# Optimization experiments

Hardware: AMD Instinct MI355X
Metric: run time of the kernel (lower is better)

Reference implementation:

```python
import jax, jax.numpy as jnp
import numpy as np

EPS = 1e-5
K = 3  # kernel size
K2 = K * K
PAD = 1


def conv2d(x, w, b):
    # x: [B,C,H,W], w: [O,C,3,3], b: [O]
    y = jax.lax.conv_general_dilated(
        x, w, window_strides=(1, 1), padding=((PAD, PAD), (PAD, PAD)),
        dimension_numbers=("NCHW", "OIHW", "NCHW"))
    return y + b[None, :, None, None]


def bilinear_sample(x, py, px):
    # x: [B,C,H,W]; py,px: [B,K2,H,W] fractional sample coords (zero pad outside)
    B, C, H, W = x.shape
    y0 = jnp.floor(py)
    x0 = jnp.floor(px)
    wy1 = py - y0
    wx1 = px - x0
    wy0 = 1.0 - wy1
    wx0 = 1.0 - wx1
    xf = x.reshape(B, C, H * W)

    def gather(yy, xx):
        valid = ((yy >= 0) & (yy < H) & (xx >= 0) & (xx < W)).astype(x.dtype)
        yc = jnp.clip(yy, 0, H - 1).astype(jnp.int32)
        xc = jnp.clip(xx, 0, W - 1).astype(jnp.int32)
        idx = yc * W + xc  # [B,K2,H,W]
        v = jax.vmap(lambda f, i: f[:, i])(xf, idx)  # [B,C,K2,H,W]
        return v * valid[:, None]

    out = (wy0 * wx0)[:, None] * gather(y0, x0)
    out = out + (wy0 * wx1)[:, None] * gather(y0, x0 + 1)
    out = out + (wy1 * wx0)[:, None] * gather(y0 + 1, x0)
    out = out + (wy1 * wx1)[:, None] * gather(y0 + 1, x0 + 1)
    return out  # [B,C,K2,H,W]


def deform_conv2d(x, offset_w, offset_b, w, b):
    # Deformable conv v1: offsets predicted by a plain 3x3 conv, then
    # bilinear gather at (base grid + kernel tap + learned offset),
    # contracted against the conv weight.
    B, C, H, W = x.shape
    O = w.shape[0]
    off = conv2d(x, offset_w, offset_b)            # [B, 2*K2, H, W]
    off = off.reshape(B, K2, 2, H, W)
    dy, dx = off[:, :, 0], off[:, :, 1]            # [B,K2,H,W]
    ky = (jnp.arange(K2) // K - PAD).astype(x.dtype)[None, :, None, None]
    kx = (jnp.arange(K2) % K - PAD).astype(x.dtype)[None, :, None, None]
    ii = jnp.arange(H, dtype=x.dtype)[None, None, :, None]
    jj = jnp.arange(W, dtype=x.dtype)[None, None, None, :]
    py = ii + ky + dy
    px = jj + kx + dx
    sampled = bilinear_sample(x, py, px)           # [B,C,K2,H,W]
    out = jnp.einsum("bckhw,ock->bohw", sampled, w.reshape(O, C, K2))
    return out + b[None, :, None, None]


def group_norm(x, gamma, beta):
    # num_groups=1: normalize over (C,H,W) per sample
    mean = jnp.mean(x, axis=(1, 2, 3), keepdims=True)
    var = jnp.var(x, axis=(1, 2, 3), keepdims=True)
    xn = (x - mean) * jax.lax.rsqrt(var + EPS)
    return xn * gamma[None, :, None, None] + beta[None, :, None, None]


def setup_inputs() -> dict:
    key = jax.random.key(0)
    ks = jax.random.split(key, 8)
    B, C, H, W = 4, 256, 64, 64
    s = 1.0 / np.sqrt(C * K2)
    inp = {
        "x": jax.random.normal(ks[0], (B, C, H, W), jnp.float32),
        "ow1": jax.random.normal(ks[1], (2 * K2, C, K, K), jnp.float32) * 0.01,
        "ob1": jnp.zeros((2 * K2,), jnp.float32),
        "dw1": jax.random.normal(ks[2], (C, C, K, K), jnp.float32) * s,
        "db1": jax.random.normal(ks[3], (C,), jnp.float32) * 0.01,
        "g1": jnp.ones((C,), jnp.float32),
        "b1": jnp.zeros((C,), jnp.float32),
        "ow2": jax.random.normal(ks[4], (2 * K2, C, K, K), jnp.float32) * 0.01,
        "ob2": jnp.zeros((2 * K2,), jnp.float32),
        "dw2": jax.random.normal(ks[5], (C, C, K, K), jnp.float32) * s,
        "db2": jax.random.normal(ks[6], (C,), jnp.float32) * 0.01,
        "g2": jnp.ones((C,), jnp.float32),
        "b2": jnp.zeros((C,), jnp.float32),
        "g3": jnp.ones((C,), jnp.float32),
        "b3": jnp.zeros((C,), jnp.float32),
    }
    return inp


def reference(x, ow1, ob1, dw1, db1, g1, b1,
              ow2, ob2, dw2, db2, g2, b2, g3, b3):
    # block: deform_conv -> GN -> relu -> (dropout=id in eval) x2
    h = jax.nn.relu(group_norm(deform_conv2d(x, ow1, ob1, dw1, db1), g1, b1))
    h = jax.nn.relu(group_norm(deform_conv2d(h, ow2, ob2, dw2, db2), g2, b2))
    # drop_path=0 -> identity; in_channels == out_channels -> identity shortcut
    return group_norm(h + x, g3, b3)
```

## Files before the change

kernel.cpp:

```cpp
#include <hip/hip_runtime.h>
#include <hip/hip_fp16.h>

constexpr int B = 4, C = 256, H = 64, W = 64, HW = 4096;
constexpr int K2 = 9, OFFC = 18;
constexpr int SSTR = 296;

typedef short s16x8 __attribute__((ext_vector_type(8)));
typedef float f32x4 __attribute__((ext_vector_type(4)));

__device__ __forceinline__ unsigned short f2bf(float f) {
  unsigned u = __float_as_uint(f);
  u += 0x7fffu + ((u >> 16) & 1u);
  return (unsigned short)(u >> 16);
}
__device__ __forceinline__ float bflo(unsigned q) { return __uint_as_float(q << 16); }
__device__ __forceinline__ float bfhi(unsigned q) { return __uint_as_float(q & 0xffff0000u); }

__global__ void cvt_bf16_reord_k(const float* __restrict__ src, unsigned short* __restrict__ dst) {
  int idx = blockIdx.x * 256 + threadIdx.x;
  if (idx >= 256 * 2304) return;
  int o = idx / 2304, kap = idx % 2304;
  int cbi = kap / 288, rem = kap % 288;
  int k = rem >> 5, c = rem & 31;
  dst[idx] = f2bf(src[((size_t)(o * 256 + cbi * 32 + c)) * 9 + k]);
}

__launch_bounds__(256)
__global__ void offset_conv_k(const float* __restrict__ x, const float* __restrict__ ow,
                              const float* __restrict__ ob, float* __restrict__ off4) {
  int cq = blockIdx.x & 3;
  int i  = (blockIdx.x >> 2) & 63;
  int b  = blockIdx.x >> 8;
  int t = threadIdx.x;
  int j = t & 63;
  int ocg = __builtin_amdgcn_readfirstlane(t >> 6);
  __shared__ float xs[32][3][66];
  const float* xb = x + (size_t)b * C * HW;

  if (t < 96) { int cc = t & 31, rr = t >> 5; xs[cc][rr][0] = 0.f; xs[cc][rr][65] = 0.f; }

  float acc[5];
#pragma unroll
  for (int s = 0; s < 5; ++s) {
    int oc = ocg + 4 * s;
    acc[s] = (cq == 0 && oc < OFFC) ? ob[oc] : 0.f;
  }

  for (int half = 0; half < 2; ++half) {
    int cbase = cq * 64 + half * 32;
    for (int idx = t; idx < 32 * 192; idx += 256) {
      int cc = idx / 192, rem = idx - cc * 192;
      int rr = rem >> 6, j2 = rem & 63;
      int yy = i + rr - 1;
      xs[cc][rr][1 + j2] = (yy >= 0 && yy < H) ? xb[(size_t)(cbase + cc) * HW + yy * 64 + j2] : 0.f;
    }
    __syncthreads();
    for (int cc = 0; cc < 32; ++cc) {
      float xv[9];
#pragma unroll
      for (int rr = 0; rr < 3; ++rr)
#pragma unroll
        for (int dxx = 0; dxx < 3; ++dxx) xv[rr * 3 + dxx] = xs[cc][rr][j + dxx];
#pragma unroll
      for (int s = 0; s < 5; ++s) {
        int oc = ocg + 4 * s;
        if (oc < OFFC) {
          const float* wp = ow + ((size_t)oc * C + cbase + cc) * 9;
#pragma unroll
          for (int k = 0; k < 9; ++k) acc[s] += xv[k] * wp[k];
        }
      }
    }
    __syncthreads();
  }
#pragma unroll
  for (int s = 0; s < 5; ++s) {
    int oc = ocg + 4 * s;
    if (oc < OFFC)
      off4[(((size_t)(cq * B + b) * OFFC + oc) << 12) + (i << 6) + j] = acc[s];
  }
}

__launch_bounds__(512, 4)
__global__ void deform_mfma_k(const float* __restrict__ xin, const float* __restrict__ off4,
                              const unsigned short* __restrict__ wbf,
                              const float* __restrict__ bias,
                              float* __restrict__ y, float* __restrict__ stats) {
  int jh = blockIdx.x & 1;
  int i  = (blockIdx.x >> 1) & 63;
  int b  = blockIdx.x >> 7;
  int t = threadIdx.x;
  int lane = t & 63, wv = t >> 6;
  int cidx = lane & 15, r = lane >> 4;
  int jl = t & 31, cg = t >> 5;

  __shared__ __align__(16) unsigned s_md[K2][32][4];
  __shared__ __align__(16) unsigned short s_pt[2][11264];
  __shared__ __align__(16) unsigned short s_s[32][SSTR];
  __shared__ float rs_[8], rq_[8];

  const float* xb = xin + (size_t)b * C * HW;
  int br = i - 3, bc = (jh << 5) - 5;

  int gof[11], wof[11];
#pragma unroll
  for (int e = 0; e < 11; ++e) {
    int pos = jl + (e << 5);
    int row = pos / 44, col = pos - row * 44;
    int rr = min(max(br + row, 0), H - 1);
    int c2 = min(max(bc + col, 0), W - 1);
    gof[e] = rr * 64 + c2;
    wof[e] = cg * 704 + row * 88 + col * 2;
  }

  float l0[11], l1[11];
  {
    const float* bp = xb + (size_t)(cg * 2) * HW;
#pragma unroll
    for (int e = 0; e < 11; ++e) { l0[e] = bp[gof[e]]; l1[e] = bp[HW + gof[e]]; }
  }

  for (int idx = t; idx < K2 * 32; idx += 512) {
    int k = idx >> 5, jj = idx & 31;
    int j = (jh << 5) + jj;
    float dy = 0.f, dx = 0.f;
#pragma unroll
    for (int cq = 0; cq < 4; ++cq) {
      const float* p = off4 + (((size_t)(cq * B + b) * OFFC) << 12) + (i << 6) + j;
      dy += p[(2 * k) << 12];
      dx += p[(2 * k + 1) << 12];
    }
    float py = (float)(i + (k / 3) - 1) + dy;
    float px = (float)(j + (k % 3) - 1) + dx;
    float y0f = floorf(py), x0f = floorf(px);
    float wy1 = py - y0f, wx1 = px - x0f;
    float wy0 = 1.f - wy1, wx0 = 1.f - wx1;
    int y0 = (int)y0f, x0 = (int)x0f;
    if (y0 < 0 || y0 >= H)         wy0 = 0.f;
    if (y0 + 1 < 0 || y0 + 1 >= H) wy1 = 0.f;
    if (x0 < 0 || x0 >= W)         wx0 = 0.f;
    if (x0 + 1 < 0 || x0 + 1 >= W) wx1 = 0.f;
    int y0c = min(max(y0, 0), H - 1), y1c = min(max(y0 + 1, 0), H - 1);
    int x0c = min(max(x0, 0), W - 1), x1c = min(max(x0 + 1, 0), W - 1);
    int dys = y1c - y0c, dxs = x1c - x0c;
    unsigned p0 = (unsigned)__half_as_ushort(__float2half_rn(wy0 * wx0)) |
                  ((unsigned)__half_as_ushort(__float2half_rn(wy0 * wx1)) << 16);
    unsigned p1 = (unsigned)__half_as_ushort(__float2half_rn(wy1 * wx0)) |
                  ((unsigned)__half_as_ushort(__float2half_rn(wy1 * wx1)) << 16);
    bool ip = (y0c >= br) && (y1c <= br + 7) && (x0c >= bc) && (x1c <= bc + 43);
    unsigned pb = (unsigned)((y0c - br) * 88 + (x0c - bc) * 2);
    unsigned p2 = (ip ? (pb & 0xfff) : 0u) | ((unsigned)dxs << 12) | ((unsigned)dys << 13) |
                  (ip ? 0u : 0x4000u);
    unsigned p3 = (unsigned)(y0c * 64 + x0c) | ((unsigned)dxs << 12) | ((unsigned)dys << 13);
    *reinterpret_cast<uint4*>(&s_md[k][jj][0]) = make_uint4(p0, p1, p2, p3);
  }

#pragma unroll
  for (int e = 0; e < 11; ++e)
    *reinterpret_cast<unsigned*>(&s_pt[0][wof[e]]) =
        (unsigned)f2bf(l0[e]) | ((unsigned)f2bf(l1[e]) << 16);
  __syncthreads();

  f32x4 acc[2][2];
#pragma unroll
  for (int m = 0; m < 2; ++m) {
    acc[m][0] = {0.f, 0.f, 0.f, 0.f};
    acc[m][1] = {0.f, 0.f, 0.f, 0.f};
  }
  int ob_ = wv * 32;
  const unsigned short* w0p = wbf + (size_t)(ob_ + cidx) * 2304;
  const unsigned short* w1p = w0p + 16 * 2304;

  for (int cb = 0; cb < 8; ++cb) {
    int cur = cb & 1;
    if (cb < 7) {
      const float* bp = xb + (size_t)((cb + 1) * 32 + cg * 2) * HW;
#pragma unroll
      for (int e = 0; e < 11; ++e) { l0[e] = bp[gof[e]]; l1[e] = bp[HW + gof[e]]; }
    }
    {
      const unsigned short* pt = &s_pt[cur][cg * 704];
#pragma unroll
      for (int k = 0; k < K2; ++k) {
        uint4 m = *reinterpret_cast<const uint4*>(&s_md[k][jl][0]);
        float w00 = __half2float(__ushort_as_half((unsigned short)(m.x & 0xffff)));
        float w01 = __half2float(__ushort_as_half((unsigned short)(m.x >> 16)));
        float w10 = __half2float(__ushort_as_half((unsigned short)(m.y & 0xffff)));
        float w11 = __half2float(__ushort_as_half((unsigned short)(m.y >> 16)));
        int pb = m.z & 0xfff;
        int dx2 = ((m.z >> 12) & 1) * 2, dy88 = ((m.z >> 13) & 1) * 88;
        unsigned q00 = *reinterpret_cast<const unsigned*>(pt + pb);
        unsigned q01 = *reinterpret_cast<const unsigned*>(pt + pb + dx2);
        unsigned q10 = *reinterpret_cast<const unsigned*>(pt + pb + dy88);
        unsigned q11 = *reinterpret_cast<const unsigned*>(pt + pb + dy88 + dx2);
        float v0 = w00 * bflo(q00) + w01 * bflo(q01) + w10 * bflo(q10) + w11 * bflo(q11);
        float v1 = w00 * bfhi(q00) + w01 * bfhi(q01) + w10 * bfhi(q10) + w11 * bfhi(q11);
        if (m.z & 0x4000u) {
          int i00 = m.w & 0xfff;
          int fdx = (m.w >> 12) & 1, fdy = ((m.w >> 13) & 1) * 64;
          const float* xc0 = xb + (size_t)(cb * 32 + cg * 2) * HW;
          const float* xc1 = xc0 + HW;
          v0 = w00 * xc0[i00] + w01 * xc0[i00 + fdx] + w10 * xc0[i00 + fdy] + w11 * xc0[i00 + fdy + fdx];
          v1 = w00 * xc1[i00] + w01 * xc1[i00 + fdx] + w10 * xc1[i00 + fdy] + w11 * xc1[i00 + fdy + fdx];
        }
        *reinterpret_cast<unsigned*>(&s_s[jl][k * 32 + cg * 2]) =
            (unsigned)f2bf(v0) | ((unsigned)f2bf(v1) << 16);
      }
    }
    if (cb < 7) {
#pragma unroll
      for (int e = 0; e < 11; ++e)
        *reinterpret_cast<unsigned*>(&s_pt[cur ^ 1][wof[e]]) =
            (unsigned)f2bf(l0[e]) | ((unsigned)f2bf(l1[e]) << 16);
    }
    __syncthreads();
    int kb0 = cb * 288 + r * 8;
#pragma unroll 3
    for (int kk = 0; kk < 9; ++kk) {
      int kl = kk * 32 + r * 8;
      s16x8 a0 = *(const s16x8*)&s_s[cidx][kl];
      s16x8 a1 = *(const s16x8*)&s_s[16 + cidx][kl];
      s16x8 b0 = *(const s16x8*)&w0p[kb0 + kk * 32];
      s16x8 b1 = *(const s16x8*)&w1p[kb0 + kk * 32];
      acc[0][0] = __builtin_amdgcn_mfma_f32_16x16x32_bf16(a0, b0, acc[0][0], 0, 0, 0);
      acc[1][0] = __builtin_amdgcn_mfma_f32_16x16x32_bf16(a1, b0, acc[1][0], 0, 0, 0);
      acc[0][1] = __builtin_amdgcn_mfma_f32_16x16x32_bf16(a0, b1, acc[0][1], 0, 0, 0);
      acc[1][1] = __builtin_amdgcn_mfma_f32_16x16x32_bf16(a1, b1, acc[1][1], 0, 0, 0);
    }
    __syncthreads();
  }

  float bv0 = bias[ob_ + cidx], bv1 = bias[ob_ + 16 + cidx];
  float psum = 0.f, psq = 0.f;
#pragma unroll
  for (int m = 0; m < 2; ++m) {
#pragma unroll
    for (int n = 0; n < 2; ++n) {
      int o = ob_ + n * 16 + cidx;
      float bv = n ? bv1 : bv0;
      float4 vv;
      vv.x = acc[m][n][0] + bv; vv.y = acc[m][n][1] + bv;
      vv.z = acc[m][n][2] + bv; vv.w = acc[m][n][3] + bv;
      *reinterpret_cast<float4*>(y + (((size_t)(b * C + o)) << 12) + (i << 6) + (jh << 5) + m * 16 + r * 4) = vv;
      psum += vv.x + vv.y + vv.z + vv.w;
      psq  += vv.x * vv.x + vv.y * vv.y + vv.z * vv.z + vv.w * vv.w;
    }
  }
#pragma unroll
  for (int d = 32; d > 0; d >>= 1) {
    psum += __shfl_down(psum, d);
    psq  += __shfl_down(psq, d);
  }
  if (lane == 0) { rs_[wv] = psum; rq_[wv] = psq; }
  __syncthreads();
  if (t == 0) {
    float a = 0.f, s2 = 0.f;
    for (int u = 0; u < 8; ++u) { a += rs_[u]; s2 += rq_[u]; }
    atomicAdd(&stats[b * 2],     a);
    atomicAdd(&stats[b * 2 + 1], s2);
  }
}

__global__ void gn_k(const float* __restrict__ yv, const float* __restrict__ stats,
                     const float* __restrict__ g, const float* __restrict__ be,
                     float* __restrict__ outp, int relu) {
  const float inv = 1.f / (float)(C * HW);
  int stride = gridDim.x * blockDim.x;
  int total4 = B * C * HW / 4;
  for (int idx = blockIdx.x * blockDim.x + threadIdx.x; idx < total4; idx += stride) {
    int e = idx << 2;
    int b = e >> 20;
    int c = (e >> 12) & 255;
    float mean = stats[b * 2] * inv;
    float var  = stats[b * 2 + 1] * inv - mean * mean;
    float rs   = rsqrtf(var + 1e-5f);
    float a  = g[c] * rs;
    float b2 = be[c] - mean * a;
    float4 v = *reinterpret_cast<const float4*>(yv + e);
    float4 rr;
    rr.x = v.x * a + b2; rr.y = v.y * a + b2; rr.z = v.z * a + b2; rr.w = v.w * a + b2;
    if (relu) {
      rr.x = fmaxf(0.f, rr.x); rr.y = fmaxf(0.f, rr.y);
      rr.z = fmaxf(0.f, rr.z); rr.w = fmaxf(0.f, rr.w);
    }
    *reinterpret_cast<float4*>(outp + e) = rr;
  }
}

__global__ void res_stats_k(const float* __restrict__ h2, const float* __restrict__ x,
                            float* __restrict__ z, float* __restrict__ stats) {
  int b = blockIdx.x >> 8;
  int seg = blockIdx.x & 255;
  size_t base = ((size_t)b << 20) + ((size_t)seg << 12);
  int t = threadIdx.x;
  float psum = 0.f, psq = 0.f;
#pragma unroll
  for (int u = 0; u < 4; ++u) {
    size_t e = base + (size_t)(u * 256 + t) * 4;
    float4 a = *reinterpret_cast<const float4*>(h2 + e);
    float4 c = *reinterpret_cast<const float4*>(x + e);
    float4 rr = make_float4(a.x + c.x, a.y + c.y, a.z + c.z, a.w + c.w);
    *reinterpret_cast<float4*>(z + e) = rr;
    psum += rr.x + rr.y + rr.z + rr.w;
    psq  += rr.x * rr.x + rr.y * rr.y + rr.z * rr.z + rr.w * rr.w;
  }
#pragma unroll
  for (int d = 32; d > 0; d >>= 1) {
    psum += __shfl_down(psum, d);
    psq  += __shfl_down(psq, d);
  }
  __shared__ float rs_[4], rq_[4];
  int wid = t >> 6, lane = t & 63;
  if (lane == 0) { rs_[wid] = psum; rq_[wid] = psq; }
  __syncthreads();
  if (t == 0) {
    float a = 0.f, s2 = 0.f;
    for (int u = 0; u < 4; ++u) { a += rs_[u]; s2 += rq_[u]; }
    atomicAdd(&stats[b * 2],     a);
    atomicAdd(&stats[b * 2 + 1], s2);
  }
}

extern "C" void kernel_launch(void* const* d_in, const int* in_sizes, int n_in,
                              void* d_out, int out_size, void* d_ws, size_t ws_size,
                              hipStream_t stream) {
  const float* x   = (const float*)d_in[0];
  const float* ow1 = (const float*)d_in[1];
  const float* ob1 = (const float*)d_in[2];
  const float* dw1 = (const float*)d_in[3];
  const float* db1 = (const float*)d_in[4];
  const float* g1  = (const float*)d_in[5];
  const float* b1  = (const float*)d_in[6];
  const float* ow2 = (const float*)d_in[7];
  const float* ob2 = (const float*)d_in[8];
  const float* dw2 = (const float*)d_in[9];
  const float* db2 = (const float*)d_in[10];
  const float* g2  = (const float*)d_in[11];
  const float* b2  = (const float*)d_in[12];
  const float* g3  = (const float*)d_in[13];
  const float* b3  = (const float*)d_in[14];

  float* ws   = (float*)d_ws;
  float* off4 = ws;
  float* yb   = ws + 1179648;
  float* hb   = ws + 1179648 + 4194304;
  float* st   = ws + 1179648 + 2 * 4194304;
  unsigned short* wbf1 = (unsigned short*)(ws + 9568288);
  unsigned short* wbf2 = (unsigned short*)(ws + 9568288 + 294912);
  float* outp = (float*)d_out;

  hipMemsetAsync(st, 0, 32 * sizeof(float), stream);
  cvt_bf16_reord_k<<<2304, 256, 0, stream>>>(dw1, wbf1);
  cvt_bf16_reord_k<<<2304, 256, 0, stream>>>(dw2, wbf2);

  offset_conv_k<<<1024, 256, 0, stream>>>(x, ow1, ob1, off4);
  deform_mfma_k<<<512, 512, 0, stream>>>(x, off4, wbf1, db1, yb, st + 0);
  gn_k<<<2048, 256, 0, stream>>>(yb, st + 0, g1, b1, hb, 1);
  offset_conv_k<<<1024, 256, 0, stream>>>(hb, ow2, ob2, off4);
  deform_mfma_k<<<512, 512, 0, stream>>>(hb, off4, wbf2, db2, yb, st + 8);
  gn_k<<<2048, 256, 0, stream>>>(yb, st + 8, g2, b2, hb, 1);
  res_stats_k<<<1024, 256, 0, stream>>>(hb, x, yb, st + 16);
  gn_k<<<2048, 256, 0, stream>>>(yb, st + 16, g3, b3, outp, 0);
}
```

Baseline: 474.0 us.

## Switch activations to packed fp16 channel pairs and fuse GN with residual

Activations are now stored as packed half2 channel pairs (x converted once, hidden h written packed by a GN+ReLU kernel). The offset conv and the bilinear sampling use packed half2 FMA, and the MFMA moves from bf16 to f16. The second GN+ReLU is fused with the residual add and the stats pass. This cuts memory traffic and ALU work in the sampling and offset conv, at the cost of fp16 range and precision in the offset conv accumulation and the bilinear interpolation.

```diff
diff --git a/kernel.cpp b/kernel.cpp
--- a/kernel.cpp
+++ b/kernel.cpp
@@ -3,30 +3,46 @@
 
 constexpr int B = 4, C = 256, H = 64, W = 64, HW = 4096;
 constexpr int K2 = 9, OFFC = 18;
-constexpr int SSTR = 296;
-
-typedef short s16x8 __attribute__((ext_vector_type(8)));
+constexpr int PSTR = 356;
+
+typedef _Float16 f16x8 __attribute__((ext_vector_type(8)));
 typedef float f32x4 __attribute__((ext_vector_type(4)));
 
-__device__ __forceinline__ unsigned short f2bf(float f) {
-  unsigned u = __float_as_uint(f);
-  u += 0x7fffu + ((u >> 16) & 1u);
-  return (unsigned short)(u >> 16);
-}
-__device__ __forceinline__ float bflo(unsigned q) { return __uint_as_float(q << 16); }
-__device__ __forceinline__ float bfhi(unsigned q) { return __uint_as_float(q & 0xffff0000u); }
-
-__global__ void cvt_bf16_reord_k(const float* __restrict__ src, unsigned short* __restrict__ dst) {
+__device__ __forceinline__ __half2 u2h(unsigned u) { return *reinterpret_cast<__half2*>(&u); }
+__device__ __forceinline__ unsigned h2u(__half2 h) { return *reinterpret_cast<unsigned*>(&h); }
+__device__ __forceinline__ unsigned packh2(float a, float b) {
+  __half2 h = __floats2half2_rn(a, b);
+  return *reinterpret_cast<unsigned*>(&h);
+}
+
+__global__ void cvt_wf16_reord_k(const float* __restrict__ src, __half* __restrict__ dst) {
   int idx = blockIdx.x * 256 + threadIdx.x;
   if (idx >= 256 * 2304) return;
   int o = idx / 2304, kap = idx % 2304;
   int cbi = kap / 288, rem = kap % 288;
   int k = rem >> 5, c = rem & 31;
-  dst[idx] = f2bf(src[((size_t)(o * 256 + cbi * 32 + c)) * 9 + k]);
+  dst[idx] = __float2half_rn(src[((size_t)(o * 256 + cbi * 32 + c)) * 9 + k]);
+}
+
+__global__ void cvt_owpair_k(const float* __restrict__ src, unsigned* __restrict__ dst) {
+  int idx = blockIdx.x * 256 + threadIdx.x;
+  if (idx >= OFFC * 128 * 9) return;
+  int k = idx % 9, cp = (idx / 9) & 127, oc = idx / 1152;
+  dst[idx] = packh2(src[((size_t)oc * 256 + 2 * cp) * 9 + k],
+                    src[((size_t)oc * 256 + 2 * cp + 1) * 9 + k]);
+}
+
+__global__ void cvt_xpair_k(const float* __restrict__ src, unsigned* __restrict__ dst) {
+  int idx = blockIdx.x * 256 + threadIdx.x;
+  int px4 = idx & 1023, c2 = (idx >> 10) & 127, b = idx >> 17;
+  const float4 v0 = *reinterpret_cast<const float4*>(src + (((size_t)(b * 256 + 2 * c2)) << 12) + px4 * 4);
+  const float4 v1 = *reinterpret_cast<const float4*>(src + (((size_t)(b * 256 + 2 * c2 + 1)) << 12) + px4 * 4);
+  uint4 o = make_uint4(packh2(v0.x, v1.x), packh2(v0.y, v1.y), packh2(v0.z, v1.z), packh2(v0.w, v1.w));
+  *reinterpret_cast<uint4*>(dst + (((size_t)(b * 128 + c2)) << 12) + px4 * 4) = o;
 }
 
 __launch_bounds__(256)
-__global__ void offset_conv_k(const float* __restrict__ x, const float* __restrict__ ow,
+__global__ void offset_conv_k(const unsigned* __restrict__ xp, const unsigned* __restrict__ owp,
                               const float* __restrict__ ob, float* __restrict__ off4) {
   int cq = blockIdx.x & 3;
   int i  = (blockIdx.x >> 2) & 63;
@@ -34,10 +50,19 @@
   int t = threadIdx.x;
   int j = t & 63;
   int ocg = __builtin_amdgcn_readfirstlane(t >> 6);
-  __shared__ float xs[32][3][66];
-  const float* xb = x + (size_t)b * C * HW;
-
-  if (t < 96) { int cc = t & 31, rr = t >> 5; xs[cc][rr][0] = 0.f; xs[cc][rr][65] = 0.f; }
+  __shared__ unsigned xs[32][3][66];
+  const unsigned* xb = xp + (size_t)b * 128 * HW;
+
+  for (int pos = t; pos < 32 * 3 * 66; pos += 256) {
+    int c = pos % 66, rp = pos / 66;
+    int rr = rp % 3, p = rp / 3;
+    int yy = i + rr - 1, xx = c - 1;
+    unsigned v = 0;
+    if (yy >= 0 && yy < H && xx >= 0 && xx < W)
+      v = xb[(size_t)(cq * 32 + p) * HW + yy * 64 + xx];
+    xs[p][rr][c] = v;
+  }
+  __syncthreads();
 
   float acc[5];
 #pragma unroll
@@ -46,32 +71,24 @@
     acc[s] = (cq == 0 && oc < OFFC) ? ob[oc] : 0.f;
   }
 
-  for (int half = 0; half < 2; ++half) {
-    int cbase = cq * 64 + half * 32;
-    for (int idx = t; idx < 32 * 192; idx += 256) {
-      int cc = idx / 192, rem = idx - cc * 192;
-      int rr = rem >> 6, j2 = rem & 63;
-      int yy = i + rr - 1;
-      xs[cc][rr][1 + j2] = (yy >= 0 && yy < H) ? xb[(size_t)(cbase + cc) * HW + yy * 64 + j2] : 0.f;
-    }
-    __syncthreads();
-    for (int cc = 0; cc < 32; ++cc) {
-      float xv[9];
-#pragma unroll
-      for (int rr = 0; rr < 3; ++rr)
-#pragma unroll
-        for (int dxx = 0; dxx < 3; ++dxx) xv[rr * 3 + dxx] = xs[cc][rr][j + dxx];
-#pragma unroll
-      for (int s = 0; s < 5; ++s) {
-        int oc = ocg + 4 * s;
-        if (oc < OFFC) {
-          const float* wp = ow + ((size_t)oc * C + cbase + cc) * 9;
-#pragma unroll
-          for (int k = 0; k < 9; ++k) acc[s] += xv[k] * wp[k];
-        }
+  for (int p = 0; p < 32; ++p) {
+    __half2 xv[9];
+#pragma unroll
+    for (int rr = 0; rr < 3; ++rr)
+#pragma unroll
+      for (int dxx = 0; dxx < 3; ++dxx) xv[rr * 3 + dxx] = u2h(xs[p][rr][j + dxx]);
+#pragma unroll
+    for (int s = 0; s < 5; ++s) {
+      int oc = ocg + 4 * s;
+      if (oc < OFFC) {
+        const unsigned* wp = owp + ((size_t)oc * 128 + cq * 32 + p) * 9;
+        __half2 h = __floats2half2_rn(0.f, 0.f);
+#pragma unroll
+        for (int k = 0; k < 9; ++k) h = __hfma2(xv[k], u2h(wp[k]), h);
+        float2 f = __half22float2(h);
+        acc[s] += f.x + f.y;
       }
     }
-    __syncthreads();
   }
 #pragma unroll
   for (int s = 0; s < 5; ++s) {
@@ -82,8 +99,8 @@
 }
 
 __launch_bounds__(512, 4)
-__global__ void deform_mfma_k(const float* __restrict__ xin, const float* __restrict__ off4,
-                              const unsigned short* __restrict__ wbf,
+__global__ void deform_mfma_k(const unsigned* __restrict__ xp, const float* __restrict__ off4,
+                              const __half* __restrict__ wf,
                               const float* __restrict__ bias,
                               float* __restrict__ y, float* __restrict__ stats) {
   int jh = blockIdx.x & 1;
@@ -95,11 +112,12 @@
   int jl = t & 31, cg = t >> 5;
 
   __shared__ __align__(16) unsigned s_md[K2][32][4];
-  __shared__ __align__(16) unsigned short s_pt[2][11264];
-  __shared__ __align__(16) unsigned short s_s[32][SSTR];
+  __shared__ __align__(8)  unsigned s_mf[K2][32][2];
+  __shared__ unsigned s_pt[2][16 * PSTR];
+  __shared__ __align__(16) unsigned s_su[32][148];
   __shared__ float rs_[8], rq_[8];
 
-  const float* xb = xin + (size_t)b * C * HW;
+  const unsigned* xb = xp + (size_t)b * 128 * HW;
   int br = i - 3, bc = (jh << 5) - 5;
 
   int gof[11], wof[11];
@@ -110,14 +128,14 @@
     int rr = min(max(br + row, 0), H - 1);
     int c2 = min(max(bc + col, 0), W - 1);
     gof[e] = rr * 64 + c2;
-    wof[e] = cg * 704 + row * 88 + col * 2;
-  }
-
-  float l0[11], l1[11];
+    wof[e] = row * 44 + col;
+  }
+
+  unsigned l[11];
   {
-    const float* bp = xb + (size_t)(cg * 2) * HW;
-#pragma unroll
-    for (int e = 0; e < 11; ++e) { l0[e] = bp[gof[e]]; l1[e] = bp[HW + gof[e]]; }
+    const unsigned* bp = xb + (size_t)cg * HW;
+#pragma unroll
+    for (int e = 0; e < 11; ++e) l[e] = bp[gof[e]];
   }
 
   for (int idx = t; idx < K2 * 32; idx += 512) {
@@ -143,23 +161,29 @@
     int y0c = min(max(y0, 0), H - 1), y1c = min(max(y0 + 1, 0), H - 1);
     int x0c = min(max(x0, 0), W - 1), x1c = min(max(x0 + 1, 0), W - 1);
     int dys = y1c - y0c, dxs = x1c - x0c;
-    unsigned p0 = (unsigned)__half_as_ushort(__float2half_rn(wy0 * wx0)) |
-                  ((unsigned)__half_as_ushort(__float2half_rn(wy0 * wx1)) << 16);
-    unsigned p1 = (unsigned)__half_as_ushort(__float2half_rn(wy1 * wx0)) |
-                  ((unsigned)__half_as_ushort(__float2half_rn(wy1 * wx1)) << 16);
+    uint4 wq;
+    wq.x = h2u(__float2half2_rn(wy0 * wx0));
+    wq.y = h2u(__float2half2_rn(wy0 * wx1));
+    wq.z = h2u(__float2half2_rn(wy1 * wx0));
+    wq.w = h2u(__float2half2_rn(wy1 * wx1));
+    *reinterpret_cast<uint4*>(&s_md[k][jj][0]) = wq;
     bool ip = (y0c >= br) && (y1c <= br + 7) && (x0c >= bc) && (x1c <= bc + 43);
-    unsigned pb = (unsigned)((y0c - br) * 88 + (x0c - bc) * 2);
-    unsigned p2 = (ip ? (pb & 0xfff) : 0u) | ((unsigned)dxs << 12) | ((unsigned)dys << 13) |
-                  (ip ? 0u : 0x4000u);
-    unsigned p3 = (unsigned)(y0c * 64 + x0c) | ((unsigned)dxs << 12) | ((unsigned)dys << 13);
-    *reinterpret_cast<uint4*>(&s_md[k][jj][0]) = make_uint4(p0, p1, p2, p3);
-  }
-
-#pragma unroll
-  for (int e = 0; e < 11; ++e)
-    *reinterpret_cast<unsigned*>(&s_pt[0][wof[e]]) =
-        (unsigned)f2bf(l0[e]) | ((unsigned)f2bf(l1[e]) << 16);
+    unsigned pb = (unsigned)((y0c - br) * 44 + (x0c - bc));
+    s_mf[k][jj][0] = (ip ? (pb & 0xfff) : 0u) | ((unsigned)dxs << 12) | ((unsigned)dys << 13) |
+                     (ip ? 0u : 0x4000u);
+    s_mf[k][jj][1] = (unsigned)(y0c * 64 + x0c) | ((unsigned)dxs << 12) | ((unsigned)dys << 13);
+  }
+
+#pragma unroll
+  for (int e = 0; e < 11; ++e) s_pt[0][cg * PSTR + wof[e]] = l[e];
   __syncthreads();
+
+  unsigned pbf[9], fbk[9];
+#pragma unroll
+  for (int k = 0; k < K2; ++k) {
+    uint2 mm = *reinterpret_cast<const uint2*>(&s_mf[k][jl][0]);
+    pbf[k] = mm.x; fbk[k] = mm.y;
+  }
 
   f32x4 acc[2][2];
 #pragma unroll
@@ -168,64 +192,59 @@
     acc[m][1] = {0.f, 0.f, 0.f, 0.f};
   }
   int ob_ = wv * 32;
-  const unsigned short* w0p = wbf + (size_t)(ob_ + cidx) * 2304;
-  const unsigned short* w1p = w0p + 16 * 2304;
+  const __half* w0p = wf + (size_t)(ob_ + cidx) * 2304;
+  const __half* w1p = w0p + 16 * 2304;
 
   for (int cb = 0; cb < 8; ++cb) {
     int cur = cb & 1;
     if (cb < 7) {
-      const float* bp = xb + (size_t)((cb + 1) * 32 + cg * 2) * HW;
-#pragma unroll
-      for (int e = 0; e < 11; ++e) { l0[e] = bp[gof[e]]; l1[e] = bp[HW + gof[e]]; }
+      const unsigned* bp = xb + (size_t)((cb + 1) * 16 + cg) * HW;
+#pragma unroll
+      for (int e = 0; e < 11; ++e) l[e] = bp[gof[e]];
     }
     {
-      const unsigned short* pt = &s_pt[cur][cg * 704];
+      const unsigned* pt = &s_pt[cur][cg * PSTR];
 #pragma unroll
       for (int k = 0; k < K2; ++k) {
         uint4 m = *reinterpret_cast<const uint4*>(&s_md[k][jl][0]);
-        float w00 = __half2float(__ushort_as_half((unsigned short)(m.x & 0xffff)));
-        float w01 = __half2float(__ushort_as_half((unsigned short)(m.x >> 16)));
-        float w10 = __half2float(__ushort_as_half((unsigned short)(m.y & 0xffff)));
-        float w11 = __half2float(__ushort_as_half((unsigned short)(m.y >> 16)));
-        int pb = m.z & 0xfff;
-        int dx2 = ((m.z >> 12) & 1) * 2, dy88 = ((m.z >> 13) & 1) * 88;
-        unsigned q00 = *reinterpret_cast<const unsigned*>(pt + pb);
-        unsigned q01 = *reinterpret_cast<const unsigned*>(pt + pb + dx2);
-        unsigned q10 = *reinterpret_cast<const unsigned*>(pt + pb + dy88);
-        unsigned q11 = *reinterpret_cast<const unsigned*>(pt + pb + dy88 + dx2);
-        float v0 = w00 * bflo(q00) + w01 * bflo(q01) + w10 * bflo(q10) + w11 * bflo(q11);
-        float v1 = w00 * bfhi(q00) + w01 * bfhi(q01) + w10 * bfhi(q10) + w11 * bfhi(q11);
-        if (m.z & 0x4000u) {
-          int i00 = m.w & 0xfff;
-          int fdx = (m.w >> 12) & 1, fdy = ((m.w >> 13) & 1) * 64;
-          const float* xc0 = xb + (size_t)(cb * 32 + cg * 2) * HW;
-          const float* xc1 = xc0 + HW;
-          v0 = w00 * xc0[i00] + w01 * xc0[i00 + fdx] + w10 * xc0[i00 + fdy] + w11 * xc0[i00 + fdy + fdx];
-          v1 = w00 * xc1[i00] + w01 * xc1[i00 + fdx] + w10 * xc1[i00 + fdy] + w11 * xc1[i00 + fdy + fdx];
+        unsigned z = pbf[k];
+        int pb = z & 0xfff;
+        int dxx = (z >> 12) & 1, dyy = ((z >> 13) & 1) ? 44 : 0;
+        __half2 q00 = u2h(pt[pb]),        q01 = u2h(pt[pb + dxx]);
+        __half2 q10 = u2h(pt[pb + dyy]),  q11 = u2h(pt[pb + dyy + dxx]);
+        __half2 v = __hmul2(u2h(m.x), q00);
+        v = __hfma2(u2h(m.y), q01, v);
+        v = __hfma2(u2h(m.z), q10, v);
+        v = __hfma2(u2h(m.w), q11, v);
+        if (z & 0x4000u) {
+          unsigned f = fbk[k];
+          int i00 = f & 0xfff;
+          int fdx = (f >> 12) & 1, fdy = ((f >> 13) & 1) ? 64 : 0;
+          const unsigned* xc = xb + (size_t)(cb * 16 + cg) * HW;
+          v = __hmul2(u2h(m.x), u2h(xc[i00]));
+          v = __hfma2(u2h(m.y), u2h(xc[i00 + fdx]), v);
+          v = __hfma2(u2h(m.z), u2h(xc[i00 + fdy]), v);
+          v = __hfma2(u2h(m.w), u2h(xc[i00 + fdy + fdx]), v);
         }
-        *reinterpret_cast<unsigned*>(&s_s[jl][k * 32 + cg * 2]) =
-            (unsigned)f2bf(v0) | ((unsigned)f2bf(v1) << 16);
+        s_su[jl][k * 16 + cg] = h2u(v);
       }
     }
     if (cb < 7) {
 #pragma unroll
-      for (int e = 0; e < 11; ++e)
-        *reinterpret_cast<unsigned*>(&s_pt[cur ^ 1][wof[e]]) =
-            (unsigned)f2bf(l0[e]) | ((unsigned)f2bf(l1[e]) << 16);
+      for (int e = 0; e < 11; ++e) s_pt[cur ^ 1][cg * PSTR + wof[e]] = l[e];
     }
     __syncthreads();
     int kb0 = cb * 288 + r * 8;
 #pragma unroll 3
     for (int kk = 0; kk < 9; ++kk) {
-      int kl = kk * 32 + r * 8;
-      s16x8 a0 = *(const s16x8*)&s_s[cidx][kl];
-      s16x8 a1 = *(const s16x8*)&s_s[16 + cidx][kl];
-      s16x8 b0 = *(const s16x8*)&w0p[kb0 + kk * 32];
-      s16x8 b1 = *(const s16x8*)&w1p[kb0 + kk * 32];
-      acc[0][0] = __builtin_amdgcn_mfma_f32_16x16x32_bf16(a0, b0, acc[0][0], 0, 0, 0);
-      acc[1][0] = __builtin_amdgcn_mfma_f32_16x16x32_bf16(a1, b0, acc[1][0], 0, 0, 0);
-      acc[0][1] = __builtin_amdgcn_mfma_f32_16x16x32_bf16(a0, b1, acc[0][1], 0, 0, 0);
-      acc[1][1] = __builtin_amdgcn_mfma_f32_16x16x32_bf16(a1, b1, acc[1][1], 0, 0, 0);
+      f16x8 a0 = *(const f16x8*)&s_su[cidx][kk * 16 + r * 4];
+      f16x8 a1 = *(const f16x8*)&s_su[16 + cidx][kk * 16 + r * 4];
+      f16x8 b0 = *(const f16x8*)&w0p[kb0 + kk * 32];
+      f16x8 b1 = *(const f16x8*)&w1p[kb0 + kk * 32];
+      acc[0][0] = __builtin_amdgcn_mfma_f32_16x16x32_f16(a0, b0, acc[0][0], 0, 0, 0);
+      acc[1][0] = __builtin_amdgcn_mfma_f32_16x16x32_f16(a1, b0, acc[1][0], 0, 0, 0);
+      acc[0][1] = __builtin_amdgcn_mfma_f32_16x16x32_f16(a0, b1, acc[0][1], 0, 0, 0);
+      acc[1][1] = __builtin_amdgcn_mfma_f32_16x16x32_f16(a1, b1, acc[1][1], 0, 0, 0);
     }
     __syncthreads();
   }
@@ -261,9 +280,76 @@
   }
 }
 
+__global__ void gn_pair_k(const float* __restrict__ yv, const float* __restrict__ stats,
+                          const float* __restrict__ g, const float* __restrict__ be,
+                          unsigned* __restrict__ outp) {
+  const float inv = 1.f / (float)(C * HW);
+  int idx = blockIdx.x * 256 + threadIdx.x;
+  int px4 = idx & 1023, c2 = (idx >> 10) & 127, b = idx >> 17;
+  float mean = stats[b * 2] * inv;
+  float var  = stats[b * 2 + 1] * inv - mean * mean;
+  float rs   = rsqrtf(var + 1e-5f);
+  float a0 = g[2 * c2] * rs,     bb0 = be[2 * c2] - mean * a0;
+  float a1 = g[2 * c2 + 1] * rs, bb1 = be[2 * c2 + 1] - mean * a1;
+  const float4 v0 = *reinterpret_cast<const float4*>(yv + (((size_t)(b * 256 + 2 * c2)) << 12) + px4 * 4);
+  const float4 v1 = *reinterpret_cast<const float4*>(yv + (((size_t)(b * 256 + 2 * c2 + 1)) << 12) + px4 * 4);
+  uint4 o;
+  o.x = packh2(fmaxf(0.f, v0.x * a0 + bb0), fmaxf(0.f, v1.x * a1 + bb1));
+  o.y = packh2(fmaxf(0.f, v0.y * a0 + bb0), fmaxf(0.f, v1.y * a1 + bb1));
+  o.z = packh2(fmaxf(0.f, v0.z * a0 + bb0), fmaxf(0.f, v1.z * a1 + bb1));
+  o.w = packh2(fmaxf(0.f, v0.w * a0 + bb0), fmaxf(0.f, v1.w * a1 + bb1));
+  *reinterpret_cast<uint4*>(outp + (((size_t)(b * 128 + c2)) << 12) + px4 * 4) = o;
+}
+
+__global__ void gn2res_k(const float* __restrict__ yv, const float* __restrict__ stats,
+                         const float* __restrict__ g, const float* __restrict__ be,
+                         const float* __restrict__ x, float* __restrict__ z,
+                         float* __restrict__ stats3) {
+  const float inv = 1.f / (float)(C * HW);
+  int b = blockIdx.x >> 8;
+  int seg = blockIdx.x & 255;
+  size_t base = ((size_t)b << 20) + ((size_t)seg << 12);
+  int t = threadIdx.x;
+  float mean = stats[b * 2] * inv;
+  float var  = stats[b * 2 + 1] * inv - mean * mean;
+  float rsv  = rsqrtf(var + 1e-5f);
+  int c = seg;
+  float a = g[c] * rsv, bb = be[c] - mean * a;
+  float psum = 0.f, psq = 0.f;
+#pragma unroll
+  for (int u = 0; u < 4; ++u) {
+    size_t e = base + (size_t)(u * 256 + t) * 4;
+    float4 v = *reinterpret_cast<const float4*>(yv + e);
+    float4 xr = *reinterpret_cast<const float4*>(x + e);
+    float4 rr;
+    rr.x = fmaxf(0.f, v.x * a + bb) + xr.x;
+    rr.y = fmaxf(0.f, v.y * a + bb) + xr.y;
+    rr.z = fmaxf(0.f, v.z * a + bb) + xr.z;
+    rr.w = fmaxf(0.f, v.w * a + bb) + xr.w;
+    *reinterpret_cast<float4*>(z + e) = rr;
+    psum += rr.x + rr.y + rr.z + rr.w;
+    psq  += rr.x * rr.x + rr.y * rr.y + rr.z * rr.z + rr.w * rr.w;
+  }
+#pragma unroll
+  for (int d = 32; d > 0; d >>= 1) {
+    psum += __shfl_down(psum, d);
+    psq  += __shfl_down(psq, d);
+  }
+  __shared__ float rs_[4], rq_[4];
+  int wid = t >> 6, lane = t & 63;
+  if (lane == 0) { rs_[wid] = psum; rq_[wid] = psq; }
+  __syncthreads();
+  if (t == 0) {
+    float aa = 0.f, s2 = 0.f;
+    for (int u = 0; u < 4; ++u) { aa += rs_[u]; s2 += rq_[u]; }
+    atomicAdd(&stats3[b * 2],     aa);
+    atomicAdd(&stats3[b * 2 + 1], s2);
+  }
+}
+
 __global__ void gn_k(const float* __restrict__ yv, const float* __restrict__ stats,
                      const float* __restrict__ g, const float* __restrict__ be,
-                     float* __restrict__ outp, int relu) {
+                     float* __restrict__ outp) {
   const float inv = 1.f / (float)(C * HW);
   int stride = gridDim.x * blockDim.x;
   int total4 = B * C * HW / 4;
@@ -279,45 +365,7 @@
     float4 v = *reinterpret_cast<const float4*>(yv + e);
     float4 rr;
     rr.x = v.x * a + b2; rr.y = v.y * a + b2; rr.z = v.z * a + b2; rr.w = v.w * a + b2;
-    if (relu) {
-      rr.x = fmaxf(0.f, rr.x); rr.y = fmaxf(0.f, rr.y);
-      rr.z = fmaxf(0.f, rr.z); rr.w = fmaxf(0.f, rr.w);
-    }
     *reinterpret_cast<float4*>(outp + e) = rr;
-  }
-}
-
-__global__ void res_stats_k(const float* __restrict__ h2, const float* __restrict__ x,
-                            float* __restrict__ z, float* __restrict__ stats) {
-  int b = blockIdx.x >> 8;
-  int seg = blockIdx.x & 255;
-  size_t base = ((size_t)b << 20) + ((size_t)seg << 12);
-  int t = threadIdx.x;
-  float psum = 0.f, psq = 0.f;
-#pragma unroll
-  for (int u = 0; u < 4; ++u) {
-    size_t e = base + (size_t)(u * 256 + t) * 4;
-    float4 a = *reinterpret_cast<const float4*>(h2 + e);
-    float4 c = *reinterpret_cast<const float4*>(x + e);
-    float4 rr = make_float4(a.x + c.x, a.y + c.y, a.z + c.z, a.w + c.w);
-    *reinterpret_cast<float4*>(z + e) = rr;
-    psum += rr.x + rr.y + rr.z + rr.w;
-    psq  += rr.x * rr.x + rr.y * rr.y + rr.z * rr.z + rr.w * rr.w;
-  }
-#pragma unroll
-  for (int d = 32; d > 0; d >>= 1) {
-    psum += __shfl_down(psum, d);
-    psq  += __shfl_down(psq, d);
-  }
-  __shared__ float rs_[4], rq_[4];
-  int wid = t >> 6, lane = t & 63;
-  if (lane == 0) { rs_[wid] = psum; rq_[wid] = psq; }
-  __syncthreads();
-  if (t == 0) {
-    float a = 0.f, s2 = 0.f;
-    for (int u = 0; u < 4; ++u) { a += rs_[u]; s2 += rq_[u]; }
-    atomicAdd(&stats[b * 2],     a);
-    atomicAdd(&stats[b * 2 + 1], s2);
   }
 }
 
@@ -343,22 +391,27 @@
   float* ws   = (float*)d_ws;
   float* off4 = ws;
   float* yb   = ws + 1179648;
-  float* hb   = ws + 1179648 + 4194304;
-  float* st   = ws + 1179648 + 2 * 4194304;
-  unsigned short* wbf1 = (unsigned short*)(ws + 9568288);
-  unsigned short* wbf2 = (unsigned short*)(ws + 9568288 + 294912);
+  float* st   = ws + 1179648 + 4194304;
+  unsigned* xh = (unsigned*)(ws + 5373984);
+  unsigned* hh = (unsigned*)(ws + 7471136);
+  __half* wf1 = (__half*)(ws + 9568288);
+  __half* wf2 = (__half*)(ws + 9863200);
+  unsigned* owp1 = (unsigned*)(ws + 10158112);
+  unsigned* owp2 = (unsigned*)(ws + 10178848);
   float* outp = (float*)d_out;
 
   hipMemsetAsync(st, 0, 32 * sizeof(float), stream);
-  cvt_bf16_reord_k<<<2304, 256, 0, stream>>>(dw1, wbf1);
-  cvt_bf16_reord_k<<<2304, 256, 0, stream>>>(dw2, wbf2);
-
-  offset_conv_k<<<1024, 256, 0, stream>>>(x, ow1, ob1, off4);
-  deform_mfma_k<<<512, 512, 0, stream>>>(x, off4, wbf1, db1, yb, st + 0);
-  gn_k<<<2048, 256, 0, stream>>>(yb, st + 0, g1, b1, hb, 1);
-  offset_conv_k<<<1024, 256, 0, stream>>>(hb, ow2, ob2, off4);
-  deform_mfma_k<<<512, 512, 0, stream>>>(hb, off4, wbf2, db2, yb, st + 8);
-  gn_k<<<2048, 256, 0, stream>>>(yb, st + 8, g2, b2, hb, 1);
-  res_stats_k<<<1024, 256, 0, stream>>>(hb, x, yb, st + 16);
-  gn_k<<<2048, 256, 0, stream>>>(yb, st + 16, g3, b3, outp, 0);
-}
+  cvt_wf16_reord_k<<<2304, 256, 0, stream>>>(dw1, wf1);
+  cvt_wf16_reord_k<<<2304, 256, 0, stream>>>(dw2, wf2);
+  cvt_owpair_k<<<81, 256, 0, stream>>>(ow1, owp1);
+  cvt_owpair_k<<<81, 256, 0, stream>>>(ow2, owp2);
+  cvt_xpair_k<<<2048, 256, 0, stream>>>(x, xh);
+
+  offset_conv_k<<<1024, 256, 0, stream>>>(xh, owp1, ob1, off4);
+  deform_mfma_k<<<512, 512, 0, stream>>>(xh, off4, wf1, db1, yb, st + 0);
+  gn_pair_k<<<2048, 256, 0, stream>>>(yb, st + 0, g1, b1, hh);
+  offset_conv_k<<<1024, 256, 0, stream>>>(hh, owp2, ob2, off4);
+  deform_mfma_k<<<512, 512, 0, stream>>>(hh, off4, wf2, db2, yb, st + 8);
+  gn2res_k<<<1024, 256, 0, stream>>>(yb, st + 8, g2, b2, x, yb, st + 16);
+  gn_k<<<2048, 256, 0, stream>>>(yb, st + 16, g3, b3, outp);
+}
```

Measured after the change: 765.9 us. 1.62x slower.
